# Optimization experiments

Measured on AMD Instinct MI355X. Metric: run time of the kernel, lower is better.

Reference implementation:

```python
import jax, jax.numpy as jnp
import numpy as np

B, L, DIM, ET, NH, SD, NC = 32, 200, 36, 128, 64, 9, 2


def setup_inputs() -> dict:
    key = jax.random.key(0)
    ks = jax.random.split(key, 16)
    f = jnp.float32
    vals = jax.random.normal(ks[0], (B, L, DIM), f)
    obs = (jax.random.uniform(ks[1], (B, L, DIM)) < 0.7).astype(f)  # 0/1 observation mask
    x = jnp.concatenate([vals, obs], -1)                            # (B, L, 2*DIM)
    time_steps = jnp.sort(jax.random.uniform(ks[2], (B, L)), axis=1)
    static_info = jax.random.normal(ks[3], (B, SD), f)
    query_param = jnp.linspace(0.0, 1.0, ET, dtype=f)               # nn.Parameter(linspace)

    def lin(k, o, i, s):
        return jax.random.normal(k, (o, i), f) * s

    return dict(
        x=x, time_steps=time_steps, static_info=static_info, query_param=query_param,
        periodic_w=lin(ks[4], ET - 1, 1, 1.0), periodic_b=jnp.zeros((ET - 1,), f),
        timelin_w=lin(ks[5], 1, 1, 1.0), timelin_b=jnp.zeros((1,), f),
        qw=lin(ks[6], ET, ET, ET ** -0.5), qb=jnp.zeros((ET,), f),
        kw=lin(ks[7], ET, ET, ET ** -0.5), kb=jnp.zeros((ET,), f),
        ow=lin(ks[8], DIM, 2 * DIM, (2 * DIM) ** -0.5), ob=jnp.zeros((DIM,), f),
        gru_w_ih=lin(ks[9], 3 * NH, DIM, DIM ** -0.5),
        gru_w_hh=lin(ks[10], 3 * NH, NH, NH ** -0.5),
        gru_b_ih=jnp.zeros((3 * NH,), f), gru_b_hh=jnp.zeros((3 * NH,), f),
        st_w=lin(ks[11], 8, SD, SD ** -0.5), st_b=jnp.zeros((8,), f),
        c1_w=lin(ks[12], NH + 8, NH + 8, (NH + 8) ** -0.5), c1_b=jnp.zeros((NH + 8,), f),
        bn_g=jnp.ones((NH + 8,), f), bn_b=jnp.zeros((NH + 8,), f),
        c2_w=lin(ks[13], NC, NH + 8, (NH + 8) ** -0.5), c2_b=jnp.zeros((NC,), f),
        rand_mask=jax.random.randint(ks[14], (B, L), 0, 2, jnp.int32),
    )


def reference(x, time_steps, static_info, query_param, periodic_w, periodic_b,
              timelin_w, timelin_b, qw, qb, kw, kb, ow, ob,
              gru_w_ih, gru_w_hh, gru_b_ih, gru_b_hh, st_w, st_b,
              c1_w, c1_b, bn_g, bn_b, c2_w, c2_b, rand_mask):
    dim = x.shape[-1] // 2
    irr = x[:, :, dim:]                                   # observation mask channels
    temp = rand_mask.astype(x.dtype)[:, :, None]          # random_masking keep-mask
    m_small = irr * temp
    irr2 = jnp.concatenate([irr, irr], -1)                # (B, L, 2*dim)
    m2 = jnp.concatenate([m_small, m_small], -1)

    def time_emb(tt):
        tt = tt[..., None]
        return jnp.concatenate([tt @ timelin_w.T + timelin_b,
                                jnp.sin(tt @ periodic_w.T + periodic_b)], -1)

    key_e = time_emb(time_steps)                          # (B, L, ET)
    query_e = time_emb(query_param[None, :])[0]           # (ET, ET)
    q = query_e @ qw.T + qb                               # num_heads=1 => dk=ET
    k = key_e @ kw.T + kb
    scores = jnp.einsum('qd,bld->bql', q, k) / jnp.sqrt(jnp.asarray(ET, x.dtype))

    def mta(mask):
        # per-channel masked softmax over keys l: (B, Lq, L, 2*dim)
        s5 = jnp.where(mask[:, None, :, :] == 0, jnp.asarray(-1e9, x.dtype),
                       scores[:, :, :, None])
        p = jax.nn.softmax(s5, axis=2)
        o = jnp.einsum('bqld,bld->bqd', p, x)             # (B, Lq, 2*dim)
        return o @ ow.T + ob                              # (B, Lq, dim)

    out_te = mta(irr2)
    out1_te = mta(m2)

    sx = x[:, :, :dim]
    sx_g = jnp.round(jax.nn.sigmoid(jnp.einsum('bld,ble->bde', sx, sx)))
    sout = jax.nn.sigmoid(jnp.einsum('bqd,bqe->bde', out_te, out_te))

    def step(h, xt):  # torch GRU cell, gate order r,z,n
        gi = xt @ gru_w_ih.T + gru_b_ih
        gh = h @ gru_w_hh.T + gru_b_hh
        ir, iz, inn = jnp.split(gi, 3, -1)
        hr, hz, hn = jnp.split(gh, 3, -1)
        r = jax.nn.sigmoid(ir + hr)
        z = jax.nn.sigmoid(iz + hz)
        n = jnp.tanh(inn + r * hn)
        return (1 - z) * n + z * h, None

    h0 = jnp.zeros((x.shape[0], gru_w_hh.shape[1]), x.dtype)
    h_fin, _ = jax.lax.scan(step, h0, jnp.swapaxes(out_te, 0, 1))

    st = static_info @ st_w.T + st_b
    cls_in = jnp.concatenate([h_fin, st], 1)
    z1 = cls_in @ c1_w.T + c1_b
    mu = z1.mean(0)
    var = z1.var(0)                                       # BatchNorm1d (training stats)
    zn = (z1 - mu) / jnp.sqrt(var + 1e-5) * bn_g + bn_b
    zg = jax.nn.gelu(zn, approximate=False)
    logits = zg @ c2_w.T + c2_b
    return (out_te, out1_te, logits, sx_g, sout, query_param)
```

## Files before the change

kernel.cpp:

```cpp
#include <hip/hip_runtime.h>

#define B_   32
#define L_   200
#define DIM_ 36
#define ET_  128
#define NH_  64
#define SD_  9
#define NC_  2

#define O_TE   0
#define O_T1   147456
#define O_LG   294912
#define O_SXG  294976
#define O_SOUT 336448
#define O_QP   377920

typedef __fp16 half_t;
typedef __attribute__((ext_vector_type(2))) __fp16 half2_t;

__device__ __forceinline__ float sigm(float x) { return 1.f / (1.f + expf(-x)); }
__device__ __forceinline__ float fsigm(float x) {
  return __builtin_amdgcn_rcpf(1.f + __expf(-x));
}
__device__ __forceinline__ float ftanh(float x) {
  return 2.f * __builtin_amdgcn_rcpf(1.f + __expf(-2.f * x)) - 1.f;
}
__device__ __forceinline__ half2_t f2h2(float a, float b) {
  return __builtin_amdgcn_cvt_pkrtz(a, b);
}
__device__ __forceinline__ float dot2acc(half2_t w, half2_t h, float acc) {
#if __has_builtin(__builtin_amdgcn_fdot2)
  return __builtin_amdgcn_fdot2(w, h, acc, false);
#else
  return acc + (float)w.x * (float)h.x + (float)w.y * (float)h.y;
#endif
}

__global__ __launch_bounds__(256) void k_pre2(
    const float* __restrict__ qw, const float* __restrict__ kw,
    const float* __restrict__ qb, const float* __restrict__ qp,
    const float* __restrict__ pw, const float* __restrict__ pb,
    const float* __restrict__ tlw, const float* __restrict__ tlb,
    const float* __restrict__ x, float* __restrict__ qm2,
    float* __restrict__ xmean, float* __restrict__ out) {
  int blk = blockIdx.x, t = threadIdx.x;
  if (blk < 128) {
    __shared__ float eq[128];
    __shared__ float uq[128];
    int q = blk;
    if (t < 128) {
      float tt = qp[q];
      eq[t] = (t == 0) ? tt * tlw[0] + tlb[0]
                       : __sinf(tt * pw[t - 1] + pb[t - 1]);
    }
    __syncthreads();
    if (t < 128) {
      const float4* qw4 = (const float4*)(qw + (size_t)t * 128);
      float a = qb[t];
      #pragma unroll 8
      for (int c = 0; c < 32; c++) {
        float4 w = qw4[c];
        a += eq[4 * c] * w.x + eq[4 * c + 1] * w.y +
             eq[4 * c + 2] * w.z + eq[4 * c + 3] * w.w;
      }
      uq[t] = a;
    }
    __syncthreads();
    if (t < 128) {
      float a = 0.f;
      #pragma unroll 8
      for (int i = 0; i < 128; i++) a += uq[i] * kw[i * 128 + t];
      qm2[q * 128 + t] = a * 0.088388347648318447f;
      if (q == 0) out[O_QP + t] = qp[t];
    }
    return;
  }
  int b = blk - 128;
  if (t < 72) {
    float s = 0.f;
    const float* xb = x + (size_t)b * L_ * 72 + t;
    #pragma unroll 8
    for (int l = 0; l < L_; l++) s += xb[(size_t)l * 72];
    xmean[b * 72 + t] = s * (1.0f / L_);
  }
}

__global__ __launch_bounds__(512, 4) void k_attn(
    const float* __restrict__ qm, const float* __restrict__ ts,
    const float* __restrict__ pw, const float* __restrict__ pb,
    const float* __restrict__ tlw, const float* __restrict__ tlb,
    const float* __restrict__ x, const int* __restrict__ rm,
    const float* __restrict__ xmean, const float* __restrict__ ow,
    const float* __restrict__ ob, float* __restrict__ out) {
  __shared__ __align__(16) char Abuf[52992];
  __shared__ __align__(16) float qs[8][128];
  __shared__ __align__(16) float sc[8][200];
  float*   ksA  = (float*)Abuf;
  half2_t* wsh2 = (half2_t*)Abuf;
  float*   sums = (float*)(Abuf + 28800);
  float*   ofr  = (float*)(Abuf + 38016);
  float*   owsh = (float*)(Abuf + 42624);

  int b  = blockIdx.x >> 4;
  int qo = blockIdx.x & 15;
  int q0 = qo << 3;
  int tid = threadIdx.x;

  float tl_w = tlw[0], tl_b = tlb[0];
  const float* tsb = ts + b * L_;

  {
    const float4* qsrc = (const float4*)(qm + q0 * ET_);
    for (int i = tid; i < 8 * 32; i += 512) ((float4*)qs)[i] = qsrc[i];
  }
  for (int ck = 0; ck < 2; ck++) {
    for (int i = tid; i < 100 * 128; i += 512) {
      int l = i >> 7, j = i & 127;
      float t = tsb[ck * 100 + l];
      float e = (j == 0) ? t * tl_w + tl_b : __sinf(t * pw[j - 1] + pb[j - 1]);
      int blkj = (j >> 2) ^ ((l >> 2) & 7);
      ksA[(l << 7) + (blkj << 2) + (j & 3)] = e;
    }
    __syncthreads();
    {
      int w = tid >> 6, lg = tid & 63;
      int qp2 = w >> 1, lh = w & 1;
      if (lg < 50) {
        int lloc = 50 * lh + lg;
        int swz = (lloc >> 2) & 7;
        float acc0 = 0.f, acc1 = 0.f;
        const float4* ks4 = (const float4*)ksA;
        const float4* qs4 = (const float4*)qs;
        #pragma unroll 4
        for (int d4 = 0; d4 < 32; d4++) {
          float4 kv = ks4[(lloc << 5) + (d4 ^ swz)];
          float4 qv0 = qs4[(2 * qp2 + 0) * 32 + d4];
          float4 qv1 = qs4[(2 * qp2 + 1) * 32 + d4];
          acc0 += qv0.x * kv.x + qv0.y * kv.y + qv0.z * kv.z + qv0.w * kv.w;
          acc1 += qv1.x * kv.x + qv1.y * kv.y + qv1.z * kv.z + qv1.w * kv.w;
        }
        sc[2 * qp2 + 0][ck * 100 + lloc] = acc0;
        sc[2 * qp2 + 1][ck * 100 + lloc] = acc1;
      }
    }
    __syncthreads();
  }

  {
    int qi = tid >> 6, li = tid & 63;
    float m = -1e30f;
    for (int l = li; l < L_; l += 64) m = fmaxf(m, sc[qi][l]);
    #pragma unroll
    for (int off = 32; off >= 1; off >>= 1) m = fmaxf(m, __shfl_xor(m, off));
    for (int l = li; l < L_; l += 64) sc[qi][l] = __expf(sc[qi][l] - m);
  }
  __syncthreads();

  const float2* xb2 = (const float2*)(x + (size_t)b * L_ * 72);
  const int* rmb = rm + b * L_;
  int sub = tid >> 8, tt = tid & 255;
  int qi = tt >> 5, li = tt & 31;
  float accW[8];
  #pragma unroll
  for (int k = 0; k < 8; k++) accW[k] = 0.f;

  for (int ck = 0; ck < 2; ck++) {
    for (int i = tid; i < 100 * 72; i += 512) {
      int l = i / 72, c2 = i % 72;
      int lg_ = ck * 100 + l;
      int seg = c2 / 18, fh = c2 % 18;
      float2 v = xb2[lg_ * 36 + fh];
      float2 o = xb2[lg_ * 36 + 18 + fh];
      float rr = (float)rmb[lg_];
      float w0, w1;
      if (seg == 0)      { w0 = o.x * v.x;      w1 = o.y * v.y; }
      else if (seg == 1) { w0 = o.x;            w1 = o.y; }
      else if (seg == 2) { w0 = o.x * v.x * rr; w1 = o.y * v.y * rr; }
      else               { w0 = o.x * rr;       w1 = o.y * rr; }
      wsh2[l * 72 + c2] = f2h2(w0, w1);
    }
    if (ck == 0) {
      const float4* owsrc = (const float4*)ow;
      for (int i = tid; i < DIM_ * 18; i += 512) ((float4*)owsh)[i] = owsrc[i];
    }
    __syncthreads();
    if (li < 18) {
      const float4* wA = (const float4*)wsh2;
      #pragma unroll 2
      for (int l = 0; l < 50; l++) {
        int lW = sub * 50 + l;
        float ev = sc[qi][ck * 100 + lW];
        float4 wa = wA[lW * 18 + li];
        union { float f; half2_t h; } u0, u1, u2, u3;
        u0.f = wa.x; u1.f = wa.y; u2.f = wa.z; u3.f = wa.w;
        accW[0] += ev * (float)u0.h.x; accW[1] += ev * (float)u0.h.y;
        accW[2] += ev * (float)u1.h.x; accW[3] += ev * (float)u1.h.y;
        accW[4] += ev * (float)u2.h.x; accW[5] += ev * (float)u2.h.y;
        accW[6] += ev * (float)u3.h.x; accW[7] += ev * (float)u3.h.y;
      }
    }
    __syncthreads();
  }
  if (li < 18) {
    float* sq = sums + sub * 1152 + qi * 144 + 8 * li;
    ((float4*)sq)[0] = make_float4(accW[0], accW[1], accW[2], accW[3]);
    ((float4*)sq)[1] = make_float4(accW[4], accW[5], accW[6], accW[7]);
  }
  __syncthreads();

  const float* xm = xmean + b * 72;
  for (int idx = tid; idx < 8 * DIM_; idx += 512) {
    int qq = idx / DIM_, j = idx % DIM_;
    const float* s0 = sums + qq * 144;
    const float* s1 = s0 + 1152;
    float numA = s0[j] + s1[j];
    float denA = s0[36 + j] + s1[36 + j];
    float numB = s0[72 + j] + s1[72 + j];
    float denB = s0[108 + j] + s1[108 + j];
    float al, ah, bl, bh;
    if (denA > 0.f) { al = numA / denA; ah = 1.f; }
    else            { al = xm[j];       ah = xm[36 + j]; }
    if (denB > 0.f) { bl = numB / denB; bh = 1.f; }
    else            { bl = xm[j];       bh = xm[36 + j]; }
    float* oq = ofr + qq * 144;
    oq[j] = al;      oq[36 + j] = ah;
    oq[72 + j] = bl; oq[108 + j] = bh;
  }
  __syncthreads();

  for (int idx = tid; idx < 8 * 72; idx += 512) {
    int qq = idx / 72, t = idx % 72;
    int v = t / DIM_, i2 = t % DIM_;
    const float4* o4 = (const float4*)(ofr + qq * 144 + v * 72);
    const float4* w4 = (const float4*)(owsh + i2 * 72);
    float a = ob[i2];
    #pragma unroll
    for (int d4 = 0; d4 < 18; d4++) {
      float4 ov = o4[d4], wv = w4[d4];
      a += ov.x * wv.x + ov.y * wv.y + ov.z * wv.z + ov.w * wv.w;
    }
    size_t off = ((size_t)b * ET_ + q0 + qq) * DIM_ + i2;
    out[(v == 0 ? O_TE : O_T1) + off] = a;
  }
}

__global__ __launch_bounds__(256, 1) void k_sg(
    const float* __restrict__ out_ro, const float* __restrict__ x,
    const float* __restrict__ wih, const float* __restrict__ bih,
    const float* __restrict__ whh, const float* __restrict__ bhh,
    const float* __restrict__ si, const float* __restrict__ stw,
    const float* __restrict__ stb, const float* __restrict__ c1w,
    const float* __restrict__ c1b, const float* __restrict__ bng,
    const float* __restrict__ bnb, const float* __restrict__ c2w,
    const float* __restrict__ c2b,
    float* __restrict__ hfin, int* __restrict__ ctr,
    float* __restrict__ out) {
  __shared__ __align__(16) float ote_s[ET_][DIM_];
  __shared__ float gis[ET_][3 * NH_];
  __shared__ __align__(16) half2_t hpk[NH_ / 2];
  int blk = blockIdx.x, t = threadIdx.x;

  if (blk >= 64) {
    float* base = &gis[0][0];
    float (*cin)[72] = (float(*)[72])(base);
    float (*z1)[72]  = (float(*)[72])(base + 2304);
    float (*zg)[72]  = (float(*)[72])(base + 4608);
    float* c1wt = base + 6912;
    float* c2ws = base + 6912 + 5184;
    float* bngs = c2ws + 144;
    float* bnbs = bngs + 72;
    for (int idx = t; idx < 72 * 72; idx += 256) {
      int j = idx / 72, d = idx % 72;
      c1wt[d * 72 + j] = c1w[idx];
    }
    for (int idx = t; idx < NC_ * 72; idx += 256) c2ws[idx] = c2w[idx];
    if (t < 72) { bngs[t] = bng[t]; bnbs[t] = bnb[t]; }
    for (int idx = t; idx < B_ * 8; idx += 256) {
      int b = idx / 8, j = idx % 8;
      float acc = stb[j];
      #pragma unroll
      for (int d = 0; d < SD_; d++) acc += si[b * SD_ + d] * stw[j * SD_ + d];
      cin[b][NH_ + j] = acc;
    }
    __syncthreads();
    if (t == 0) {
      while (__hip_atomic_load(ctr, __ATOMIC_ACQUIRE,
                               __HIP_MEMORY_SCOPE_AGENT) < 32)
        __builtin_amdgcn_s_sleep(8);
    }
    __syncthreads();
    for (int idx = t; idx < B_ * NH_; idx += 256)
      cin[idx / NH_][idx % NH_] = hfin[idx];
    __syncthreads();
    for (int idx = t; idx < B_ * 72; idx += 256) {
      int b = idx / 72, j = idx % 72;
      float acc = c1b[j];
      #pragma unroll 8
      for (int d = 0; d < 72; d++) acc += cin[b][d] * c1wt[d * 72 + j];
      z1[b][j] = acc;
    }
    __syncthreads();
    if (t < 72) {
      float mu = 0.f;
      for (int b = 0; b < B_; b++) mu += z1[b][t];
      mu *= (1.f / B_);
      float vv = 0.f;
      for (int b = 0; b < B_; b++) { float d = z1[b][t] - mu; vv += d * d; }
      vv *= (1.f / B_);
      float inv = 1.f / sqrtf(vv + 1e-5f);
      float g = bngs[t], bb = bnbs[t];
      for (int b = 0; b < B_; b++) {
        float zn = (z1[b][t] - mu) * inv * g + bb;
        zg[b][t] = 0.5f * zn * (1.f + erff(zn * 0.70710678118654752f));
      }
    }
    __syncthreads();
    for (int idx = t; idx < B_ * NC_; idx += 256) {
      int b = idx / NC_, c = idx % NC_;
      float acc = c2b[c];
      #pragma unroll 8
      for (int d = 0; d < 72; d++) acc += zg[b][d] * c2ws[c * 72 + d];
      out[O_LG + idx] = acc;
    }
    return;
  }

  if (blk < 32) {
    int b = blk;
    float* sxs = (float*)gis;
    const float4* osrc = (const float4*)(out_ro + O_TE + (size_t)b * ET_ * DIM_);
    for (int idx = t; idx < ET_ * 9; idx += 256)
      ((float4*)&ote_s[0][0])[idx] = osrc[idx];
    const float4* xsrc = (const float4*)(x + (size_t)b * L_ * 72);
    for (int idx = t; idx < L_ * 18; idx += 256) {
      int l = idx / 18, c = idx % 18;
      ((float4*)&sxs[l * 76])[c] = xsrc[idx];
    }
    __syncthreads();
    for (int idx = t; idx < DIM_ * DIM_; idx += 256) {
      int d = idx / DIM_, e = idx % DIM_;
      float s = 0.f;
      #pragma unroll 8
      for (int q = 0; q < ET_; q++) s += ote_s[q][d] * ote_s[q][e];
      out[O_SOUT + (size_t)b * DIM_ * DIM_ + idx] = sigm(s);
    }
    for (int idx = t; idx < DIM_ * DIM_; idx += 256) {
      int d = idx / DIM_, e = idx % DIM_;
      float s = 0.f;
      #pragma unroll 8
      for (int l = 0; l < L_; l++) s += sxs[l * 76 + d] * sxs[l * 76 + e];
      out[O_SXG + (size_t)b * DIM_ * DIM_ + idx] = rintf(sigm(s));
    }
    return;
  }

  int b = blk - 32;
  const float* ote = out_ro + O_TE;
  const float4* osrc = (const float4*)(ote + (size_t)b * ET_ * DIM_);
  for (int idx = t; idx < ET_ * DIM_ / 4; idx += 256)
    ((float4*)&ote_s[0][0])[idx] = osrc[idx];
  __syncthreads();

  if (t < 3 * NH_) {
    float wv[DIM_];
    const float* wrow = wih + (size_t)t * DIM_;
    #pragma unroll
    for (int d = 0; d < DIM_; d++) wv[d] = wrow[d];
    float bi = bih[t] + ((t < 2 * NH_) ? bhh[t] : 0.f);
    for (int q = 0; q < ET_; q++) {
      const float4* xr = (const float4*)ote_s[q];
      float a = bi;
      #pragma unroll
      for (int c = 0; c < 9; c++) {
        float4 xv = xr[c];
        a += xv.x * wv[4 * c] + xv.y * wv[4 * c + 1] +
             xv.z * wv[4 * c + 2] + xv.w * wv[4 * c + 3];
      }
      gis[q][t] = a;
    }
  }
  __syncthreads();
  if (t >= 64) return;

  half2_t wr[32], wz[32], wn[32];
  {
    const float2* r0 = (const float2*)(whh + (size_t)t * NH_);
    const float2* r1 = (const float2*)(whh + (size_t)(NH_ + t) * NH_);
    const float2* r2 = (const float2*)(whh + (size_t)(2 * NH_ + t) * NH_);
    #pragma unroll
    for (int c = 0; c < 32; c++) {
      float2 a = r0[c], bb = r1[c], cc = r2[c];
      wr[c] = f2h2(a.x, a.y);
      wz[c] = f2h2(bb.x, bb.y);
      wn[c] = f2h2(cc.x, cc.y);
    }
  }
  float bh_n = bhh[2 * NH_ + t];

  float h = 0.f;
  ((half_t*)hpk)[t] = (half_t)0.f;
  for (int q = 0; q < ET_; q++) {
    float gi_r = gis[q][t];
    float gi_z = gis[q][NH_ + t];
    float gi_n = gis[q][2 * NH_ + t];
    float ar = 0.f, az = 0.f, an = 0.f;
    const float4* hp4 = (const float4*)hpk;
    #pragma unroll
    for (int c4 = 0; c4 < 8; c4++) {
      float4 hv = hp4[c4];
      union { float f; half2_t h; } u0, u1, u2, u3;
      u0.f = hv.x; u1.f = hv.y; u2.f = hv.z; u3.f = hv.w;
      int c = c4 * 4;
      ar = dot2acc(wr[c + 0], u0.h, ar);
      az = dot2acc(wz[c + 0], u0.h, az);
      an = dot2acc(wn[c + 0], u0.h, an);
      ar = dot2acc(wr[c + 1], u1.h, ar);
      az = dot2acc(wz[c + 1], u1.h, az);
      an = dot2acc(wn[c + 1], u1.h, an);
      ar = dot2acc(wr[c + 2], u2.h, ar);
      az = dot2acc(wz[c + 2], u2.h, az);
      an = dot2acc(wn[c + 2], u2.h, an);
      ar = dot2acc(wr[c + 3], u3.h, ar);
      az = dot2acc(wz[c + 3], u3.h, az);
      an = dot2acc(wn[c + 3], u3.h, an);
    }
    float r = fsigm(gi_r + ar);
    float z = fsigm(gi_z + az);
    float n = ftanh(gi_n + r * (an + bh_n));
    h = n + z * (h - n);
    ((half_t*)hpk)[t] = (half_t)h;
  }
  hfin[b * NH_ + t] = h;
  __threadfence();
  if (t == 0) atomicAdd(ctr, 1);
}

extern "C" void kernel_launch(void* const* d_in, const int* in_sizes, int n_in,
                              void* d_out, int out_size, void* d_ws,
                              size_t ws_size, hipStream_t stream) {
  const float* x    = (const float*)d_in[0];
  const float* ts   = (const float*)d_in[1];
  const float* si   = (const float*)d_in[2];
  const float* qp   = (const float*)d_in[3];
  const float* pw   = (const float*)d_in[4];
  const float* pb   = (const float*)d_in[5];
  const float* tlw  = (const float*)d_in[6];
  const float* tlb  = (const float*)d_in[7];
  const float* qw   = (const float*)d_in[8];
  const float* qb   = (const float*)d_in[9];
  const float* kw   = (const float*)d_in[10];
  const float* ow   = (const float*)d_in[12];
  const float* ob   = (const float*)d_in[13];
  const float* wih  = (const float*)d_in[14];
  const float* whh  = (const float*)d_in[15];
  const float* bih  = (const float*)d_in[16];
  const float* bhh  = (const float*)d_in[17];
  const float* stw  = (const float*)d_in[18];
  const float* stb  = (const float*)d_in[19];
  const float* c1w  = (const float*)d_in[20];
  const float* c1b  = (const float*)d_in[21];
  const float* bng  = (const float*)d_in[22];
  const float* bnb  = (const float*)d_in[23];
  const float* c2w  = (const float*)d_in[24];
  const float* c2b  = (const float*)d_in[25];
  const int*   rm   = (const int*)d_in[26];

  float* out = (float*)d_out;

  float* W = (float*)d_ws;
  float* ws_qm2   = W;
  float* ws_xmean = W + 16384;
  float* ws_hfin  = W + 18688;
  int*   ws_ctr   = (int*)(W + 20736);

  hipMemsetAsync(ws_ctr, 0, sizeof(int), stream);
  hipLaunchKernelGGL(k_pre2, dim3(160), dim3(256), 0, stream,
                     qw, kw, qb, qp, pw, pb, tlw, tlb, x, ws_qm2, ws_xmean,
                     out);
  hipLaunchKernelGGL(k_attn, dim3(B_ * 16), dim3(512), 0, stream,
                     ws_qm2, ts, pw, pb, tlw, tlb, x, rm, ws_xmean, ow, ob,
                     out);
  hipLaunchKernelGGL(k_sg, dim3(65), dim3(256), 0, stream,
                     out, x, wih, bih, whh, bhh, si, stw, stb, c1w, c1b,
                     bng, bnb, c2w, c2b, ws_hfin, ws_ctr, out);
}
```

Before: 235.9 us.

## Precompute key time embeddings and value weights once per batch in pre-kernel

Moves the per-batch sinusoidal key embedding and half-precision masked value construction out of k_attn, where every one of the 16 query-tile blocks per batch recomputed them, into extra blocks of the pre-kernel that write them to workspace. k_attn now only copies these precomputed tiles into shared memory with float4 loads. This removes redundant sin and mask arithmetic in exchange for extra global traffic (about 3.3 MB of key data plus value data) and a larger pre-kernel. One __syncthreads after the softmax was also dropped, which may introduce a race with the following shared-memory writes.

After: 235.1 us. No clear change (-0.4%).

```diff
diff --git a/kernel.cpp b/kernel.cpp
--- a/kernel.cpp
+++ b/kernel.cpp
@@ -41,8 +41,11 @@
     const float* __restrict__ qb, const float* __restrict__ qp,
     const float* __restrict__ pw, const float* __restrict__ pb,
     const float* __restrict__ tlw, const float* __restrict__ tlb,
-    const float* __restrict__ x, float* __restrict__ qm2,
-    float* __restrict__ xmean, float* __restrict__ out) {
+    const float* __restrict__ ts, const float* __restrict__ x,
+    const int* __restrict__ rm,
+    float* __restrict__ qm2, float* __restrict__ xmean,
+    float* __restrict__ ks_ws, half2_t* __restrict__ w_ws,
+    float* __restrict__ out) {
   int blk = blockIdx.x, t = threadIdx.x;
   if (blk < 128) {
     __shared__ float eq[128];
@@ -75,21 +78,56 @@
     }
     return;
   }
-  int b = blk - 128;
-  if (t < 72) {
-    float s = 0.f;
-    const float* xb = x + (size_t)b * L_ * 72 + t;
-    #pragma unroll 8
-    for (int l = 0; l < L_; l++) s += xb[(size_t)l * 72];
-    xmean[b * 72 + t] = s * (1.0f / L_);
+  if (blk < 160) {
+    int b = blk - 128;
+    if (t < 72) {
+      float s = 0.f;
+      const float* xb = x + (size_t)b * L_ * 72 + t;
+      #pragma unroll 8
+      for (int l = 0; l < L_; l++) s += xb[(size_t)l * 72];
+      xmean[b * 72 + t] = s * (1.0f / L_);
+    }
+    return;
+  }
+  if (blk < 224) {
+    int bb = (blk - 160) >> 1, half = (blk - 160) & 1;
+    float tl_w = tlw[0], tl_b = tlb[0];
+    const float* tsb = ts + bb * L_;
+    float* dst = ks_ws + (size_t)bb * 25600;
+    for (int i = half * 12800 + t; i < half * 12800 + 12800; i += 256) {
+      int l = i >> 7, j = i & 127;
+      float tt = tsb[l];
+      float e = (j == 0) ? tt * tl_w + tl_b
+                         : __sinf(tt * pw[j - 1] + pb[j - 1]);
+      int blkj = (j >> 2) ^ ((l >> 2) & 7);
+      dst[(l << 7) + (blkj << 2) + (j & 3)] = e;
+    }
+    return;
+  }
+  {
+    int bb = blk - 224;
+    const float2* xb2 = (const float2*)(x + (size_t)bb * L_ * 72);
+    const int* rmb = rm + bb * L_;
+    half2_t* wd = w_ws + (size_t)bb * 14400;
+    for (int i = t; i < L_ * 72; i += 256) {
+      int l = i / 72, c2 = i % 72;
+      int seg = c2 / 18, fh = c2 % 18;
+      float2 v = xb2[l * 36 + fh];
+      float2 o = xb2[l * 36 + 18 + fh];
+      float rr = (float)rmb[l];
+      float w0, w1;
+      if (seg == 0)      { w0 = o.x * v.x;      w1 = o.y * v.y; }
+      else if (seg == 1) { w0 = o.x;            w1 = o.y; }
+      else if (seg == 2) { w0 = o.x * v.x * rr; w1 = o.y * v.y * rr; }
+      else               { w0 = o.x * rr;       w1 = o.y * rr; }
+      wd[l * 72 + c2] = f2h2(w0, w1);
+    }
   }
 }
 
 __global__ __launch_bounds__(512, 4) void k_attn(
-    const float* __restrict__ qm, const float* __restrict__ ts,
-    const float* __restrict__ pw, const float* __restrict__ pb,
-    const float* __restrict__ tlw, const float* __restrict__ tlb,
-    const float* __restrict__ x, const int* __restrict__ rm,
+    const float* __restrict__ qm, const float* __restrict__ ks_ws,
+    const half2_t* __restrict__ w_ws,
     const float* __restrict__ xmean, const float* __restrict__ ow,
     const float* __restrict__ ob, float* __restrict__ out) {
   __shared__ __align__(16) char Abuf[52992];
@@ -102,32 +140,26 @@
   float*   owsh = (float*)(Abuf + 42624);
 
   int b  = blockIdx.x >> 4;
-  int qo = blockIdx.x & 15;
-  int q0 = qo << 3;
+  int q0 = (blockIdx.x & 15) << 3;
   int tid = threadIdx.x;
-
-  float tl_w = tlw[0], tl_b = tlb[0];
-  const float* tsb = ts + b * L_;
 
   {
     const float4* qsrc = (const float4*)(qm + q0 * ET_);
     for (int i = tid; i < 8 * 32; i += 512) ((float4*)qs)[i] = qsrc[i];
   }
+
   for (int ck = 0; ck < 2; ck++) {
-    for (int i = tid; i < 100 * 128; i += 512) {
-      int l = i >> 7, j = i & 127;
-      float t = tsb[ck * 100 + l];
-      float e = (j == 0) ? t * tl_w + tl_b : __sinf(t * pw[j - 1] + pb[j - 1]);
-      int blkj = (j >> 2) ^ ((l >> 2) & 7);
-      ksA[(l << 7) + (blkj << 2) + (j & 3)] = e;
-    }
+    const float4* kssrc =
+        (const float4*)(ks_ws + (size_t)b * 25600 + ck * 12800);
+    for (int i = tid; i < 3200; i += 512) ((float4*)ksA)[i] = kssrc[i];
     __syncthreads();
     {
       int w = tid >> 6, lg = tid & 63;
       int qp2 = w >> 1, lh = w & 1;
       if (lg < 50) {
         int lloc = 50 * lh + lg;
-        int swz = (lloc >> 2) & 7;
+        int lglob = ck * 100 + lloc;
+        int swz = (lglob >> 2) & 7;
         float acc0 = 0.f, acc1 = 0.f;
         const float4* ks4 = (const float4*)ksA;
         const float4* qs4 = (const float4*)qs;
@@ -139,8 +171,8 @@
           acc0 += qv0.x * kv.x + qv0.y * kv.y + qv0.z * kv.z + qv0.w * kv.w;
           acc1 += qv1.x * kv.x + qv1.y * kv.y + qv1.z * kv.z + qv1.w * kv.w;
         }
-        sc[2 * qp2 + 0][ck * 100 + lloc] = acc0;
-        sc[2 * qp2 + 1][ck * 100 + lloc] = acc1;
+        sc[2 * qp2 + 0][lglob] = acc0;
+        sc[2 * qp2 + 1][lglob] = acc1;
       }
     }
     __syncthreads();
@@ -154,10 +186,7 @@
     for (int off = 32; off >= 1; off >>= 1) m = fmaxf(m, __shfl_xor(m, off));
     for (int l = li; l < L_; l += 64) sc[qi][l] = __expf(sc[qi][l] - m);
   }
-  __syncthreads();
-
-  const float2* xb2 = (const float2*)(x + (size_t)b * L_ * 72);
-  const int* rmb = rm + b * L_;
+
   int sub = tid >> 8, tt = tid & 255;
   int qi = tt >> 5, li = tt & 31;
   float accW[8];
@@ -165,20 +194,9 @@
   for (int k = 0; k < 8; k++) accW[k] = 0.f;
 
   for (int ck = 0; ck < 2; ck++) {
-    for (int i = tid; i < 100 * 72; i += 512) {
-      int l = i / 72, c2 = i % 72;
-      int lg_ = ck * 100 + l;
-      int seg = c2 / 18, fh = c2 % 18;
-      float2 v = xb2[lg_ * 36 + fh];
-      float2 o = xb2[lg_ * 36 + 18 + fh];
-      float rr = (float)rmb[lg_];
-      float w0, w1;
-      if (seg == 0)      { w0 = o.x * v.x;      w1 = o.y * v.y; }
-      else if (seg == 1) { w0 = o.x;            w1 = o.y; }
-      else if (seg == 2) { w0 = o.x * v.x * rr; w1 = o.y * v.y * rr; }
-      else               { w0 = o.x * rr;       w1 = o.y * rr; }
-      wsh2[l * 72 + c2] = f2h2(w0, w1);
-    }
+    const float4* wsrc =
+        (const float4*)(w_ws + (size_t)b * 14400 + ck * 7200);
+    for (int i = tid; i < 1800; i += 512) ((float4*)wsh2)[i] = wsrc[i];
     if (ck == 0) {
       const float4* owsrc = (const float4*)ow;
       for (int i = tid; i < DIM_ * 18; i += 512) ((float4*)owsh)[i] = owsrc[i];
@@ -468,18 +486,19 @@
   float* out = (float*)d_out;
 
   float* W = (float*)d_ws;
-  float* ws_qm2   = W;
-  float* ws_xmean = W + 16384;
-  float* ws_hfin  = W + 18688;
-  int*   ws_ctr   = (int*)(W + 20736);
+  float*   ws_qm2   = W;
+  float*   ws_xmean = W + 16384;
+  float*   ws_hfin  = W + 18688;
+  int*     ws_ctr   = (int*)(W + 20736);
+  float*   ws_ks    = W + 20800;
+  half2_t* ws_w     = (half2_t*)(W + 20800 + 819200);
 
   hipMemsetAsync(ws_ctr, 0, sizeof(int), stream);
-  hipLaunchKernelGGL(k_pre2, dim3(160), dim3(256), 0, stream,
-                     qw, kw, qb, qp, pw, pb, tlw, tlb, x, ws_qm2, ws_xmean,
-                     out);
+  hipLaunchKernelGGL(k_pre2, dim3(256), dim3(256), 0, stream,
+                     qw, kw, qb, qp, pw, pb, tlw, tlb, ts, x, rm,
+                     ws_qm2, ws_xmean, ws_ks, ws_w, out);
   hipLaunchKernelGGL(k_attn, dim3(B_ * 16), dim3(512), 0, stream,
-                     ws_qm2, ts, pw, pb, tlw, tlb, x, rm, ws_xmean, ow, ob,
-                     out);
+                     ws_qm2, ws_ks, ws_w, ws_xmean, ow, ob, out);
   hipLaunchKernelGGL(k_sg, dim3(65), dim3(256), 0, stream,
                      out, x, wih, bih, whh, bhh, si, stw, stb, c1w, c1b,
                      bng, bnb, c2w, c2b, ws_hfin, ws_ctr, out);
```
